# Kernel optimization log

Hardware: AMD Instinct MI355X
Metric: run time of the kernel (lower is better)

## Reference

```python
import jax, jax.numpy as jnp
import numpy as np

V, H, B, T_ENC, S, T_DEC, G = 18000, 400, 16, 256, 30, 8, 3


def setup_inputs() -> dict:
    key = jax.random.key(0)
    ks = jax.random.split(key, 16)
    def n(k, shape, s=0.1):
        return jax.random.normal(k, shape, jnp.float32) * s
    return {
        'story': jax.random.randint(ks[0], (B, T_ENC), 0, V, dtype=jnp.int32),
        'target_batches': jax.random.randint(ks[1], (B, S, T_DEC), 0, V, dtype=jnp.int32),
        'emb': n(ks[2], (V, H)),
        'enc_Wih_f': n(ks[3], (3 * H, H)), 'enc_Whh_f': n(ks[4], (3 * H, H)),
        'enc_bih_f': jnp.zeros((3 * H,), jnp.float32), 'enc_bhh_f': jnp.zeros((3 * H,), jnp.float32),
        'enc_Wih_b': n(ks[5], (3 * H, H)), 'enc_Whh_b': n(ks[6], (3 * H, H)),
        'enc_bih_b': jnp.zeros((3 * H,), jnp.float32), 'enc_bhh_b': jnp.zeros((3 * H,), jnp.float32),
        'dec_Wih': n(ks[7], (3 * H, H)), 'dec_Whh': n(ks[8], (3 * H, H)),
        'dec_bih': jnp.zeros((3 * H,), jnp.float32), 'dec_bhh': jnp.zeros((3 * H,), jnp.float32),
        'W_ratio': n(ks[9], (1, 3 * H)), 'b_ratio': jnp.zeros((1,), jnp.float32),
        'W_gate': n(ks[10], (G, H)), 'b_gate': jnp.zeros((G,), jnp.float32),
        'slot_emb': n(ks[11], (S, H)),
    }


def _gru_step(h, x, Wih, Whh, bih, bhh):
    # PyTorch GRU gate order: r, z, n
    gi = x @ Wih.T + bih
    gh = h @ Whh.T + bhh
    ir, iz, ig = jnp.split(gi, 3, axis=-1)
    hr, hz, hg = jnp.split(gh, 3, axis=-1)
    r = jax.nn.sigmoid(ir + hr)
    z = jax.nn.sigmoid(iz + hz)
    g = jnp.tanh(ig + r * hg)
    return (1.0 - z) * g + z * h


def _run_gru(xs, h0, Wih, Whh, bih, bhh):
    def step(h, x):
        h2 = _gru_step(h, x, Wih, Whh, bih, bhh)
        return h2, h2
    hT, out = jax.lax.scan(step, h0, xs)
    return out, hT


def reference(story, target_batches, emb,
              enc_Wih_f, enc_Whh_f, enc_bih_f, enc_bhh_f,
              enc_Wih_b, enc_Whh_b, enc_bih_b, enc_bhh_b,
              dec_Wih, dec_Whh, dec_bih, dec_bhh,
              W_ratio, b_ratio, W_gate, b_gate, slot_emb):
    # ---- EncoderRNN (bidirectional 1-layer GRU; dropout=0 / eval mode) ----
    x = emb[story.T]                       # (T_enc, B, H)
    h0 = jnp.zeros((B, H), x.dtype)
    out_f, h_f = _run_gru(x, h0, enc_Wih_f, enc_Whh_f, enc_bih_f, enc_bhh_f)
    out_b_rev, h_b = _run_gru(x[::-1], h0, enc_Wih_b, enc_Whh_b, enc_bih_b, enc_bhh_b)
    out_b = out_b_rev[::-1]
    enc_out = jnp.transpose(out_f + out_b, (1, 0, 2))   # (B, T_enc, H) = fwd+bwd halves summed
    enc_hidden = h_f + h_b                               # (B, H)     = hidden[0] + hidden[1]

    # ---- Generator decode loop ----
    SB = S * B
    dec_in0 = jnp.broadcast_to(slot_emb[:, None, :], (S, B, H)).reshape(SB, H)
    h = jnp.tile(enc_hidden, (S, 1))                     # (SB, H)
    enc_tiled = jnp.tile(enc_out, (S, 1, 1))             # (SB, T_enc, H)
    story_tiled = jnp.tile(story, (S, 1))                # (SB, T_enc)
    rows = jnp.arange(SB)[:, None]
    # teacher-forcing tokens per step, slot-major flatten to (T_dec, SB)
    tf_tokens = jnp.transpose(target_batches, (2, 1, 0)).reshape(T_DEC, SB)

    def step(carry, tok):
        h, dec_in = carry
        h2 = _gru_step(h, dec_in, dec_Wih, dec_Whh, dec_bih, dec_bhh)  # dec_state == new hidden
        scores = jnp.einsum('nd,ntd->nt', h2, enc_tiled)               # attend (all lens == T_enc)
        prob = jax.nn.softmax(scores, axis=1)
        context = jnp.einsum('nt,ntd->nd', prob, enc_tiled)
        gate = context @ W_gate.T + b_gate                              # (SB, G)
        p_vocab = jax.nn.softmax(h2 @ emb.T, axis=1)                    # (SB, V)
        p_gen = jnp.concatenate([h2, context, dec_in], axis=-1)         # (SB, 3H)
        sw = jax.nn.sigmoid(p_gen @ W_ratio.T + b_ratio)                # (SB, 1)
        ptr = jnp.zeros((SB, V), prob.dtype).at[rows, story_tiled].add(prob)  # scatter_add copy dist
        final = (1.0 - sw) * ptr + sw * p_vocab
        dec_in_next = emb[tok]                                          # teacher forcing
        return (h2, dec_in_next), (final, gate)

    _, (finals, gates) = jax.lax.scan(step, (h, dec_in0), tf_tokens)
    all_pointer_outputs = finals.reshape(T_DEC, S, B, V).transpose(1, 2, 0, 3)  # (S, B, T_dec, V)
    all_gate_outputs = gates[0].reshape(S, B, G)                                 # gate from step 0
    return all_pointer_outputs, all_gate_outputs
```

## Files before the change

kernel.cpp:

```cpp
#include <hip/hip_runtime.h>
#include <cstdint>
#include <cstddef>

#define VV 18000
#define HH 400
#define H3 1200
#define H3P 1280
#define KP 416
#define BB 16
#define TE 256
#define SS 30
#define TDN 8
#define GGN 3
#define SBN 480
#define NROW_ENC 4096
#define VP 18048
#define MP_DEC 512

#define EBLK 25

typedef __bf16 bf16;
typedef __attribute__((ext_vector_type(8))) __bf16 bf16x8;
typedef __attribute__((ext_vector_type(4))) float f32x4;
typedef __attribute__((ext_vector_type(4))) unsigned int u32x4;

static __device__ __forceinline__ float sigf(float x) {
    return 1.0f / (1.0f + __expf(-x));
}

__global__ __launch_bounds__(256) void gemm_bt(const bf16* __restrict__ A,
                                               const bf16* __restrict__ B,
                                               float* __restrict__ C,
                                               int M, int N, int K) {
    __shared__ __align__(16) bf16 sA[128 * 32];
    __shared__ __align__(16) bf16 sB[128 * 32];
    const int tid = threadIdx.x;
    const int lane = tid & 63;
    const int wave = tid >> 6;
    const int wm = wave >> 1, wn = wave & 1;
    const int m0 = blockIdx.x * 128, n0 = blockIdx.y * 128;
    f32x4 acc[4][4] = {};
    const int c0 = tid, c1 = tid + 256;
    const int r0 = c0 >> 2, q0 = (c0 & 3) * 8;
    const int r1 = c1 >> 2, q1 = (c1 & 3) * 8;
    const int ar = lane & 15, ak = (lane >> 4) * 8;
    const int nk = K >> 5;
    for (int kt = 0; kt < nk; ++kt) {
        const int kb = kt * 32;
        uint4 a0 = *(const uint4*)(A + (size_t)(m0 + r0) * K + kb + q0);
        uint4 a1 = *(const uint4*)(A + (size_t)(m0 + r1) * K + kb + q1);
        uint4 b0 = *(const uint4*)(B + (size_t)(n0 + r0) * K + kb + q0);
        uint4 b1 = *(const uint4*)(B + (size_t)(n0 + r1) * K + kb + q1);
        __syncthreads();
        *(uint4*)(sA + r0 * 32 + q0) = a0;
        *(uint4*)(sA + r1 * 32 + q1) = a1;
        *(uint4*)(sB + r0 * 32 + q0) = b0;
        *(uint4*)(sB + r1 * 32 + q1) = b1;
        __syncthreads();
        bf16x8 af[4], bg[4];
#pragma unroll
        for (int i = 0; i < 4; ++i)
            af[i] = *(const bf16x8*)(sA + (wm * 64 + i * 16 + ar) * 32 + ak);
#pragma unroll
        for (int j = 0; j < 4; ++j)
            bg[j] = *(const bf16x8*)(sB + (wn * 64 + j * 16 + ar) * 32 + ak);
#pragma unroll
        for (int i = 0; i < 4; ++i)
#pragma unroll
            for (int j = 0; j < 4; ++j)
                acc[i][j] = __builtin_amdgcn_mfma_f32_16x16x32_bf16(af[i], bg[j], acc[i][j], 0, 0, 0);
    }
    const int cr = (lane >> 4) * 4, cc = lane & 15;
#pragma unroll
    for (int i = 0; i < 4; ++i)
#pragma unroll
        for (int j = 0; j < 4; ++j)
#pragma unroll
            for (int q = 0; q < 4; ++q) {
                int row = m0 + wm * 64 + i * 16 + cr + q;
                int col = n0 + wn * 64 + j * 16 + cc;
                C[(size_t)row * N + col] = acc[i][j][q];
            }
}

__global__ void prep_pad_bf16(const float* __restrict__ src, bf16* __restrict__ dst,
                              int rows_real, int cols_real, int rows_pad, int cols_pad) {
    int idx = blockIdx.x * blockDim.x + threadIdx.x;
    int total = rows_pad * cols_pad;
    if (idx >= total) return;
    int r = idx / cols_pad, c = idx % cols_pad;
    float v = (r < rows_real && c < cols_real) ? src[(size_t)r * cols_real + c] : 0.f;
    dst[idx] = (bf16)v;
}

__global__ void prep_aenc(const int* __restrict__ story, const float* __restrict__ emb,
                          bf16* __restrict__ dst) {
    int idx = blockIdx.x * blockDim.x + threadIdx.x;
    if (idx >= NROW_ENC * KP) return;
    int m = idx / KP, k = idx % KP;
    int t = m >> 4, b = m & 15;
    float v = 0.f;
    if (k < HH) {
        int tok = story[b * TE + t];
        v = emb[(size_t)tok * HH + k];
    }
    dst[idx] = (bf16)v;
}

__global__ void prep_decx(const int* __restrict__ target, const float* __restrict__ emb,
                          const float* __restrict__ slot, float* __restrict__ xf,
                          bf16* __restrict__ xb) {
    int idx = blockIdx.x * blockDim.x + threadIdx.x;
    if (idx >= TDN * SBN * KP) return;
    int k = idx % KP;
    int nn = idx / KP;
    int n = nn % SBN;
    int td = nn / SBN;
    int s = n >> 4, b = n & 15;
    float v = 0.f;
    if (k < HH) {
        if (td == 0) v = slot[s * HH + k];
        else {
            int tok = target[(b * SS + s) * TDN + (td - 1)];
            v = emb[(size_t)tok * HH + k];
        }
        xf[((size_t)td * SBN + n) * HH + k] = v;
    }
    xb[idx] = (bf16)v;
}

__global__ void zero_bf16k(bf16* dst, int total) {
    int idx = blockIdx.x * blockDim.x + threadIdx.x;
    if (idx < total) dst[idx] = (bf16)0.f;
}

__global__ __launch_bounds__(256) void enc_rnn5(
    const float* __restrict__ gi_f, const float* __restrict__ gi_b,
    const float* __restrict__ whh_f, const float* __restrict__ whh_b,
    const float* __restrict__ bih_f, const float* __restrict__ bhh_f,
    const float* __restrict__ bih_b, const float* __restrict__ bhh_b,
    float* __restrict__ hist_f, float* __restrict__ hist_b,
    unsigned int* __restrict__ hbuf_f, unsigned int* __restrict__ hbuf_b,
    int* __restrict__ cnt) {
    const int dir = blockIdx.x & 1;
    const int blk = blockIdx.x >> 1;
    const int j0 = blk * 16;
    const float* gi  = dir ? gi_b : gi_f;
    const float* whh = dir ? whh_b : whh_f;
    const float* bih = dir ? bih_b : bih_f;
    const float* bhh = dir ? bhh_b : bhh_f;
    float* hist = dir ? hist_b : hist_f;
    unsigned int* hbuf = dir ? hbuf_b : hbuf_f;
    int* mycnt = cnt + dir * TE;

    __shared__ float GHL[3 * 256];

    const int tid = threadIdx.x;
    const int wv = tid >> 6, lane = tid & 63;

    const int ub = tid >> 4, ucol = tid & 15;
    const int uj = j0 + ucol;
    const float bihr = bih[uj], bihz = bih[HH + uj], bihg = bih[2 * HH + uj];
    const float bhhr = bhh[uj], bhhz = bhh[HH + uj], bhhg = bhh[2 * HH + uj];

    const int kk0 = (lane >> 4) * 8;
    bf16x8 Bf[13];
    if (wv < 3) {
        const int brow = wv * HH + j0 + (lane & 15);
#pragma unroll
        for (int ks = 0; ks < 13; ++ks) {
            bf16x8 v;
#pragma unroll
            for (int e = 0; e < 8; ++e) {
                int k = kk0 + ks * 32 + e;
                v[e] = (k < HH) ? (bf16)whh[(size_t)brow * HH + k] : (bf16)0.f;
            }
            Bf[ks] = v;
        }
    }

    union UV { unsigned int d[4]; bf16x8 v; };

    float hp = 0.f;

    for (int s = 0; s < TE; ++s) {
        const int tt = dir ? (TE - 1 - s) : s;
        const float* gir = gi + ((size_t)tt * BB + ub) * H3P;
        float gi0 = gir[uj];
        float gi1 = gir[HH + uj];
        float gi2 = gir[2 * HH + uj];

        f32x4 acc0 = {}, acc1 = {};
        if (s > 0) {
            if (tid == 0) {
                while (__hip_atomic_load(&mycnt[s - 1], __ATOMIC_RELAXED,
                                         __HIP_MEMORY_SCOPE_AGENT) < EBLK)
                    __builtin_amdgcn_s_sleep(1);
            }
            __syncthreads();
            if (wv < 3) {
                const int ttp = dir ? (tt + 1) : (tt - 1);
                const unsigned int* hrow =
                    hbuf + ((size_t)ttp * BB + (lane & 15)) * KP + kk0;
                u32x4 u[13][2];
#pragma unroll
                for (int ks = 0; ks < 13; ++ks) {
                    asm volatile("global_load_dwordx4 %0, %1, off sc0 sc1"
                                 : "=v"(u[ks][0]) : "v"(hrow + ks * 32));
                    asm volatile("global_load_dwordx4 %0, %1, off sc0 sc1"
                                 : "=v"(u[ks][1]) : "v"(hrow + ks * 32 + 4));
                }
                asm volatile("s_waitcnt vmcnt(0)" ::: "memory");
                __builtin_amdgcn_sched_barrier(0);
#pragma unroll
                for (int ks = 0; ks < 13; ++ks) {
                    u32x4 a = u[ks][0], b = u[ks][1];
                    UV ah, al;
                    ah.d[0] = (a.x & 0xffffu) | (a.y << 16);
                    ah.d[1] = (a.z & 0xffffu) | (a.w << 16);
                    ah.d[2] = (b.x & 0xffffu) | (b.y << 16);
                    ah.d[3] = (b.z & 0xffffu) | (b.w << 16);
                    al.d[0] = (a.x >> 16) | (a.y & 0xffff0000u);
                    al.d[1] = (a.z >> 16) | (a.w & 0xffff0000u);
                    al.d[2] = (b.x >> 16) | (b.y & 0xffff0000u);
                    al.d[3] = (b.z >> 16) | (b.w & 0xffff0000u);
                    acc0 = __builtin_amdgcn_mfma_f32_16x16x32_bf16(ah.v, Bf[ks], acc0, 0, 0, 0);
                    acc1 = __builtin_amdgcn_mfma_f32_16x16x32_bf16(al.v, Bf[ks], acc1, 0, 0, 0);
                }
            }
        }
        if (wv < 3) {
            f32x4 at = acc0 + acc1;
            const int cb0 = wv * 256 + ((lane >> 4) * 4) * 16 + (lane & 15);
            GHL[cb0]      = at[0];
            GHL[cb0 + 16] = at[1];
            GHL[cb0 + 32] = at[2];
            GHL[cb0 + 48] = at[3];
        }
        __syncthreads();

        float ghr = GHL[tid];
        float ghz = GHL[256 + tid];
        float ghg = GHL[512 + tid];
        float r = sigf(gi0 + bihr + ghr + bhhr);
        float z = sigf(gi1 + bihz + ghz + bhhz);
        float g = tanhf(gi2 + bihg + r * (ghg + bhhg));
        float hn = (1.f - z) * g + z * hp;
        hp = hn;
        hist[((size_t)tt * BB + ub) * HH + uj] = hn;
        bf16 hi = (bf16)hn;
        bf16 lo = (bf16)(hn - (float)hi);
        unsigned int pk = (unsigned int)__builtin_bit_cast(unsigned short, hi)
                        | ((unsigned int)__builtin_bit_cast(unsigned short, lo) << 16);
        unsigned int* hw = hbuf + ((size_t)tt * BB + ub) * KP + uj;
        asm volatile("global_store_dword %0, %1, off sc0 sc1" :: "v"(hw), "v"(pk) : "memory");

        asm volatile("s_waitcnt vmcnt(0)" ::: "memory");
        __syncthreads();
        if (tid == 0)
            __hip_atomic_fetch_add(&mycnt[s], 1, __ATOMIC_RELAXED, __HIP_MEMORY_SCOPE_AGENT);
    }
}

__global__ void combine_enc(const float* __restrict__ hf, const float* __restrict__ hb,
                            float* __restrict__ enc_out) {
    int idx = blockIdx.x * blockDim.x + threadIdx.x;
    if (idx >= BB * TE * HH) return;
    int hcol = idx % HH;
    int t = (idx / HH) % TE;
    int b = idx / (HH * TE);
    size_t src = ((size_t)t * BB + b) * HH + hcol;
    enc_out[idx] = hf[src] + hb[src];
}

__global__ void init_hdec(const float* __restrict__ hf, const float* __restrict__ hb,
                          float* __restrict__ hdec) {
    int idx = blockIdx.x * blockDim.x + threadIdx.x;
    if (idx >= SBN * HH) return;
    int hcol = idx % HH;
    int n = idx / HH;
    int b = n & 15;
    hdec[idx] = hf[((size_t)(TE - 1) * BB + b) * HH + hcol] + hb[((size_t)b) * HH + hcol];
}

__global__ void conv_h(const float* __restrict__ h, bf16* __restrict__ hb) {
    int idx = blockIdx.x * blockDim.x + threadIdx.x;
    if (idx >= SBN * HH) return;
    int n = idx / HH, k = idx % HH;
    hb[(size_t)n * KP + k] = (bf16)h[idx];
}

__global__ void gru_dec(const float* __restrict__ gi, const float* __restrict__ gh,
                        const float* __restrict__ bih, const float* __restrict__ bhh,
                        const float* __restrict__ hprev, float* __restrict__ hnew) {
    int idx = blockIdx.x * blockDim.x + threadIdx.x;
    if (idx >= SBN * HH) return;
    int n = idx / HH, j = idx % HH;
    const float* gir = gi + (size_t)n * H3P;
    const float* ghr = gh + (size_t)n * H3P;
    float r = sigf(gir[j] + bih[j] + ghr[j] + bhh[j]);
    float z = sigf(gir[HH + j] + bih[HH + j] + ghr[HH + j] + bhh[HH + j]);
    float g = tanhf(gir[2 * HH + j] + bih[2 * HH + j] + r * (ghr[2 * HH + j] + bhh[2 * HH + j]));
    hnew[idx] = (1.f - z) * g + z * hprev[idx];
}

__global__ __launch_bounds__(256) void attn(const float* __restrict__ h2,
                                            const float* __restrict__ enc,
                                            float* __restrict__ prob,
                                            float* __restrict__ ctx) {
    int n = blockIdx.x, b = n & 15, tid = threadIdx.x;
    __shared__ __align__(16) float hq[HH];
    __shared__ float sc[TE];
    __shared__ float red[4];
    for (int k = tid; k < HH; k += 256) hq[k] = h2[(size_t)n * HH + k];
    __syncthreads();
    const float4* er = (const float4*)(enc + ((size_t)b * TE + tid) * HH);
    const float4* hq4 = (const float4*)hq;
    float acc = 0.f;
#pragma unroll 4
    for (int k = 0; k < HH / 4; ++k) {
        float4 e = er[k];
        float4 hv = hq4[k];
        acc += e.x * hv.x + e.y * hv.y + e.z * hv.z + e.w * hv.w;
    }
    float m = acc;
    for (int d = 32; d; d >>= 1) m = fmaxf(m, __shfl_xor(m, d));
    if ((tid & 63) == 0) red[tid >> 6] = m;
    __syncthreads();
    m = fmaxf(fmaxf(red[0], red[1]), fmaxf(red[2], red[3]));
    __syncthreads();
    float e = __expf(acc - m);
    float ssum = e;
    for (int d = 32; d; d >>= 1) ssum += __shfl_xor(ssum, d);
    if ((tid & 63) == 0) red[tid >> 6] = ssum;
    __syncthreads();
    ssum = red[0] + red[1] + red[2] + red[3];
    float p = e / ssum;
    sc[tid] = p;
    prob[(size_t)n * TE + tid] = p;
    __syncthreads();
    for (int hcol = tid; hcol < HH; hcol += 256) {
        float a = 0.f;
        for (int t = 0; t < TE; ++t) a += sc[t] * enc[((size_t)b * TE + t) * HH + hcol];
        ctx[(size_t)n * HH + hcol] = a;
    }
}

__global__ __launch_bounds__(64) void swgate(const float* __restrict__ h2,
                                             const float* __restrict__ ctx,
                                             const float* __restrict__ dx,
                                             const float* __restrict__ Wr, const float* __restrict__ br,
                                             const float* __restrict__ Wg, const float* __restrict__ bg,
                                             float* __restrict__ sw, float* __restrict__ outg,
                                             int isfirst) {
    int n = blockIdx.x, lane = threadIdx.x;
    float a = 0.f;
    for (int k = lane; k < H3; k += 64) {
        float v = (k < HH) ? h2[(size_t)n * HH + k]
                : (k < 2 * HH) ? ctx[(size_t)n * HH + (k - HH)]
                : dx[(size_t)n * HH + (k - 2 * HH)];
        a += v * Wr[k];
    }
    for (int d = 32; d; d >>= 1) a += __shfl_xor(a, d);
    if (lane == 0) sw[n] = sigf(a + br[0]);
    if (isfirst) {
        for (int g = 0; g < GGN; ++g) {
            float b2 = 0.f;
            for (int k = lane; k < HH; k += 64) b2 += ctx[(size_t)n * HH + k] * Wg[g * HH + k];
            for (int d = 32; d; d >>= 1) b2 += __shfl_xor(b2, d);
            if (lane == 0) outg[n * GGN + g] = b2 + bg[g];
        }
    }
}

__global__ __launch_bounds__(1024) void smax_final(const float* __restrict__ logits,
                                                   const float* __restrict__ sw,
                                                   float* __restrict__ out, int td) {
    int n = blockIdx.x, tid = threadIdx.x;
    __shared__ float red[16];
    __shared__ float bc[2];
    float v[18];
    float mx = -1e30f;
#pragma unroll
    for (int i = 0; i < 18; ++i) {
        int c = tid + (i << 10);
        v[i] = (c < VV) ? logits[(size_t)n * VP + c] : -1e30f;
        mx = fmaxf(mx, v[i]);
    }
    for (int d = 32; d; d >>= 1) mx = fmaxf(mx, __shfl_xor(mx, d));
    if ((tid & 63) == 0) red[tid >> 6] = mx;
    __syncthreads();
    if (tid == 0) {
        float m2 = red[0];
        for (int w = 1; w < 16; ++w) m2 = fmaxf(m2, red[w]);
        bc[0] = m2;
    }
    __syncthreads();
    mx = bc[0];
    float s = 0.f;
#pragma unroll
    for (int i = 0; i < 18; ++i) {
        int c = tid + (i << 10);
        if (c < VV) { v[i] = __expf(v[i] - mx); s += v[i]; }
    }
    for (int d = 32; d; d >>= 1) s += __shfl_xor(s, d);
    if ((tid & 63) == 0) red[tid >> 6] = s;
    __syncthreads();
    if (tid == 0) {
        float s2 = 0.f;
        for (int w = 0; w < 16; ++w) s2 += red[w];
        bc[1] = s2;
    }
    __syncthreads();
    float scale = sw[n] / bc[1];
    float* orow = out + ((size_t)n * TDN + td) * VV;
#pragma unroll
    for (int i = 0; i < 18; ++i) {
        int c = tid + (i << 10);
        if (c < VV) orow[c] = v[i] * scale;
    }
}

__global__ void scatter_ptr(const int* __restrict__ story, const float* __restrict__ prob,
                            const float* __restrict__ sw, float* __restrict__ out, int td) {
    int n = blockIdx.x, t = threadIdx.x, b = n & 15;
    int tok = story[b * TE + t];
    float val = (1.f - sw[n]) * prob[(size_t)n * TE + t];
    atomicAdd(out + ((size_t)n * TDN + td) * VV + tok, val);
}

static inline int cdiv(long long a, long long b) { return (int)((a + b - 1) / b); }

extern "C" void kernel_launch(void* const* d_in, const int* in_sizes, int n_in,
                              void* d_out, int out_size, void* d_ws, size_t ws_size,
                              hipStream_t stream) {
    const int*   story  = (const int*)d_in[0];
    const int*   target = (const int*)d_in[1];
    const float* emb    = (const float*)d_in[2];
    const float* wih_f  = (const float*)d_in[3];
    const float* whh_f  = (const float*)d_in[4];
    const float* bih_f  = (const float*)d_in[5];
    const float* bhh_f  = (const float*)d_in[6];
    const float* wih_b  = (const float*)d_in[7];
    const float* whh_b  = (const float*)d_in[8];
    const float* bih_b  = (const float*)d_in[9];
    const float* bhh_b  = (const float*)d_in[10];
    const float* dwih   = (const float*)d_in[11];
    const float* dwhh   = (const float*)d_in[12];
    const float* dbih   = (const float*)d_in[13];
    const float* dbhh   = (const float*)d_in[14];
    const float* wr     = (const float*)d_in[15];
    const float* brr    = (const float*)d_in[16];
    const float* wgg    = (const float*)d_in[17];
    const float* bgg    = (const float*)d_in[18];
    const float* slot   = (const float*)d_in[19];
    float* out = (float*)d_out;

    char* wsb = (char*)d_ws;
    size_t off = 0;
    auto alloc = [&](size_t bytes) -> char* {
        char* p = wsb + off;
        off = (off + bytes + 255) & ~(size_t)255;
        return p;
    };
    bf16*  embb  = (bf16*)alloc((size_t)VP * KP * 2);
    bf16*  aenc  = (bf16*)alloc((size_t)NROW_ENC * KP * 2);
    bf16*  wfb   = (bf16*)alloc((size_t)H3P * KP * 2);
    bf16*  wbb   = (bf16*)alloc((size_t)H3P * KP * 2);
    bf16*  dwihb = (bf16*)alloc((size_t)H3P * KP * 2);
    bf16*  dwhhb = (bf16*)alloc((size_t)H3P * KP * 2);
    bf16*  decxb = (bf16*)alloc((size_t)TDN * SBN * KP * 2);
    bf16*  h2b   = (bf16*)alloc((size_t)MP_DEC * KP * 2);
    unsigned int* hbuff = (unsigned int*)alloc((size_t)TE * BB * KP * 4);
    unsigned int* hbufb = (unsigned int*)alloc((size_t)TE * BB * KP * 4);
    float* gif   = (float*)alloc((size_t)NROW_ENC * H3P * 4);
    float* gib   = (float*)alloc((size_t)NROW_ENC * H3P * 4);
    float* gidec = (float*)alloc((size_t)TDN * SBN * H3P * 4);
    float* ghdec = (float*)alloc((size_t)MP_DEC * H3P * 4);
    float* histf = (float*)alloc((size_t)TE * BB * HH * 4);
    float* histb = (float*)alloc((size_t)TE * BB * HH * 4);
    float* encout= (float*)alloc((size_t)BB * TE * HH * 4);
    float* decxf = (float*)alloc((size_t)TDN * SBN * HH * 4);
    float* hA    = (float*)alloc((size_t)SBN * HH * 4);
    float* hB    = (float*)alloc((size_t)SBN * HH * 4);
    float* ctx   = (float*)alloc((size_t)SBN * HH * 4);
    float* probw = (float*)alloc((size_t)SBN * TE * 4);
    float* sww   = (float*)alloc((size_t)SBN * 4);
    float* logits= (float*)alloc((size_t)MP_DEC * VP * 4);
    int*   cnt   = (int*)alloc((size_t)2 * TE * 4);
    (void)ws_size; (void)in_sizes; (void)n_in; (void)out_size;

    (void)hipMemsetAsync(cnt, 0, (size_t)2 * TE * 4, stream);

    const int thr = 256;
    prep_pad_bf16<<<cdiv((long long)VP * KP, thr), thr, 0, stream>>>(emb, embb, VV, HH, VP, KP);
    prep_aenc<<<cdiv((long long)NROW_ENC * KP, thr), thr, 0, stream>>>(story, emb, aenc);
    prep_pad_bf16<<<cdiv((long long)H3P * KP, thr), thr, 0, stream>>>(wih_f, wfb, H3, HH, H3P, KP);
    prep_pad_bf16<<<cdiv((long long)H3P * KP, thr), thr, 0, stream>>>(wih_b, wbb, H3, HH, H3P, KP);
    prep_pad_bf16<<<cdiv((long long)H3P * KP, thr), thr, 0, stream>>>(dwih, dwihb, H3, HH, H3P, KP);
    prep_pad_bf16<<<cdiv((long long)H3P * KP, thr), thr, 0, stream>>>(dwhh, dwhhb, H3, HH, H3P, KP);
    prep_decx<<<cdiv((long long)TDN * SBN * KP, thr), thr, 0, stream>>>(target, emb, slot, decxf, decxb);
    zero_bf16k<<<cdiv((long long)MP_DEC * KP, thr), thr, 0, stream>>>(h2b, MP_DEC * KP);

    {
        dim3 g(NROW_ENC / 128, H3P / 128);
        gemm_bt<<<g, 256, 0, stream>>>(aenc, wfb, gif, NROW_ENC, H3P, KP);
        gemm_bt<<<g, 256, 0, stream>>>(aenc, wbb, gib, NROW_ENC, H3P, KP);
    }
    {
        dim3 g((TDN * SBN) / 128, H3P / 128);
        gemm_bt<<<g, 256, 0, stream>>>(decxb, dwihb, gidec, TDN * SBN, H3P, KP);
    }

    enc_rnn5<<<2 * EBLK, 256, 0, stream>>>(gif, gib, whh_f, whh_b,
                                           bih_f, bhh_f, bih_b, bhh_b,
                                           histf, histb, hbuff, hbufb, cnt);

    combine_enc<<<cdiv((long long)BB * TE * HH, thr), thr, 0, stream>>>(histf, histb, encout);
    init_hdec<<<cdiv((long long)SBN * HH, thr), thr, 0, stream>>>(histf, histb, hA);

    float* hc = hA;
    float* hn = hB;
    for (int td = 0; td < TDN; ++td) {
        conv_h<<<cdiv((long long)SBN * HH, thr), thr, 0, stream>>>(hc, h2b);
        {
            dim3 g(MP_DEC / 128, H3P / 128);
            gemm_bt<<<g, 256, 0, stream>>>(h2b, dwhhb, ghdec, MP_DEC, H3P, KP);
        }
        gru_dec<<<cdiv((long long)SBN * HH, thr), thr, 0, stream>>>(
            gidec + (size_t)td * SBN * H3P, ghdec, dbih, dbhh, hc, hn);
        conv_h<<<cdiv((long long)SBN * HH, thr), thr, 0, stream>>>(hn, h2b);
        attn<<<SBN, 256, 0, stream>>>(hn, encout, probw, ctx);
        swgate<<<SBN, 64, 0, stream>>>(hn, ctx, decxf + (size_t)td * SBN * HH,
                                       wr, brr, wgg, bgg, sww,
                                       out + (size_t)SBN * TDN * VV, td == 0 ? 1 : 0);
        {
            dim3 g(MP_DEC / 128, VP / 128);
            gemm_bt<<<g, 256, 0, stream>>>(h2b, embb, logits, MP_DEC, VP, KP);
        }
        smax_final<<<SBN, 1024, 0, stream>>>(logits, sww, out, td);
        scatter_ptr<<<SBN, TE, 0, stream>>>(story, probw, sww, out, td);
        float* tmp = hc; hc = hn; hn = tmp;
    }
}
```

Measured before the change: 2.025 ms.

## Replace counter-based cross-block sync with sentinel-polling on hidden-state buffer

The encoder recurrence kernel stops using a per-step atomic counter plus spin-wait to sync blocks. Instead the hidden-state exchange buffers are pre-filled with an all-ones sentinel, and each wave polls its own data loads until no sentinel remains. This removes the store-drain wait, the block barrier, the atomic increment and the separate flag poll from each of the 256 serial steps, folding sync into the data read. It relies on a packed hi/lo bf16 word never equalling 0xFFFFFFFF (a NaN pattern) and adds two large memsets of the buffers.

Measured after the change: 2.233 ms. 1.1x slower.

```diff
diff --git a/kernel.cpp b/kernel.cpp
--- a/kernel.cpp
+++ b/kernel.cpp
@@ -18,6 +18,7 @@
 #define MP_DEC 512
 
 #define EBLK 25
+#define SENT 0xFFFFFFFFu
 
 typedef __bf16 bf16;
 typedef __attribute__((ext_vector_type(8))) __bf16 bf16x8;
@@ -26,6 +27,14 @@
 
 static __device__ __forceinline__ float sigf(float x) {
     return 1.0f / (1.0f + __expf(-x));
+}
+
+static __device__ __forceinline__ unsigned umax4(unsigned m, u32x4 v) {
+    m = m > v.x ? m : v.x;
+    m = m > v.y ? m : v.y;
+    m = m > v.z ? m : v.z;
+    m = m > v.w ? m : v.w;
+    return m;
 }
 
 __global__ __launch_bounds__(256) void gemm_bt(const bf16* __restrict__ A,
@@ -134,14 +143,13 @@
     if (idx < total) dst[idx] = (bf16)0.f;
 }
 
-__global__ __launch_bounds__(256) void enc_rnn5(
+__global__ __launch_bounds__(256) void enc_rnn7(
     const float* __restrict__ gi_f, const float* __restrict__ gi_b,
     const float* __restrict__ whh_f, const float* __restrict__ whh_b,
     const float* __restrict__ bih_f, const float* __restrict__ bhh_f,
     const float* __restrict__ bih_b, const float* __restrict__ bhh_b,
     float* __restrict__ hist_f, float* __restrict__ hist_b,
-    unsigned int* __restrict__ hbuf_f, unsigned int* __restrict__ hbuf_b,
-    int* __restrict__ cnt) {
+    unsigned int* __restrict__ hbuf_f, unsigned int* __restrict__ hbuf_b) {
     const int dir = blockIdx.x & 1;
     const int blk = blockIdx.x >> 1;
     const int j0 = blk * 16;
@@ -151,7 +159,6 @@
     const float* bhh = dir ? bhh_b : bhh_f;
     float* hist = dir ? hist_b : hist_f;
     unsigned int* hbuf = dir ? hbuf_b : hbuf_f;
-    int* mycnt = cnt + dir * TE;
 
     __shared__ float GHL[3 * 256];
 
@@ -164,6 +171,7 @@
     const float bhhr = bhh[uj], bhhz = bhh[HH + uj], bhhg = bhh[2 * HH + uj];
 
     const int kk0 = (lane >> 4) * 8;
+    const bool padlane = (kk0 >= 16);
     bf16x8 Bf[13];
     if (wv < 3) {
         const int brow = wv * HH + j0 + (lane & 15);
@@ -180,6 +188,7 @@
     }
 
     union UV { unsigned int d[4]; bf16x8 v; };
+    const u32x4 zz = {0u, 0u, 0u, 0u};
 
     float hp = 0.f;
 
@@ -191,42 +200,49 @@
         float gi2 = gir[2 * HH + uj];
 
         f32x4 acc0 = {}, acc1 = {};
-        if (s > 0) {
-            if (tid == 0) {
-                while (__hip_atomic_load(&mycnt[s - 1], __ATOMIC_RELAXED,
-                                         __HIP_MEMORY_SCOPE_AGENT) < EBLK)
-                    __builtin_amdgcn_s_sleep(1);
-            }
-            __syncthreads();
-            if (wv < 3) {
-                const int ttp = dir ? (tt + 1) : (tt - 1);
-                const unsigned int* hrow =
-                    hbuf + ((size_t)ttp * BB + (lane & 15)) * KP + kk0;
-                u32x4 u[13][2];
+        if (s > 0 && wv < 3) {
+            const int ttp = dir ? (tt + 1) : (tt - 1);
+            const unsigned int* hrow =
+                hbuf + ((size_t)ttp * BB + (lane & 15)) * KP + kk0;
+            u32x4 ua[13], ubv[13];
+            while (true) {
 #pragma unroll
                 for (int ks = 0; ks < 13; ++ks) {
-                    asm volatile("global_load_dwordx4 %0, %1, off sc0 sc1"
-                                 : "=v"(u[ks][0]) : "v"(hrow + ks * 32));
-                    asm volatile("global_load_dwordx4 %0, %1, off sc0 sc1"
-                                 : "=v"(u[ks][1]) : "v"(hrow + ks * 32 + 4));
+                    asm volatile("global_load_dwordx4 %0, %1, off offset:%c2 sc0 sc1"
+                                 : "=v"(ua[ks]) : "v"(hrow), "n"(ks * 128));
+                    asm volatile("global_load_dwordx4 %0, %1, off offset:%c2 sc0 sc1"
+                                 : "=v"(ubv[ks]) : "v"(hrow), "n"(ks * 128 + 16));
                 }
                 asm volatile("s_waitcnt vmcnt(0)" ::: "memory");
                 __builtin_amdgcn_sched_barrier(0);
-#pragma unroll
-                for (int ks = 0; ks < 13; ++ks) {
-                    u32x4 a = u[ks][0], b = u[ks][1];
-                    UV ah, al;
-                    ah.d[0] = (a.x & 0xffffu) | (a.y << 16);
-                    ah.d[1] = (a.z & 0xffffu) | (a.w << 16);
-                    ah.d[2] = (b.x & 0xffffu) | (b.y << 16);
-                    ah.d[3] = (b.z & 0xffffu) | (b.w << 16);
-                    al.d[0] = (a.x >> 16) | (a.y & 0xffff0000u);
-                    al.d[1] = (a.z >> 16) | (a.w & 0xffff0000u);
-                    al.d[2] = (b.x >> 16) | (b.y & 0xffff0000u);
-                    al.d[3] = (b.z >> 16) | (b.w & 0xffff0000u);
-                    acc0 = __builtin_amdgcn_mfma_f32_16x16x32_bf16(ah.v, Bf[ks], acc0, 0, 0, 0);
-                    acc1 = __builtin_amdgcn_mfma_f32_16x16x32_bf16(al.v, Bf[ks], acc1, 0, 0, 0);
+                unsigned mx = 0u;
+#pragma unroll
+                for (int ks = 0; ks < 12; ++ks) {
+                    mx = umax4(mx, ua[ks]);
+                    mx = umax4(mx, ubv[ks]);
                 }
+                if (!padlane) {
+                    mx = umax4(mx, ua[12]);
+                    mx = umax4(mx, ubv[12]);
+                }
+                if (__all((int)(mx != SENT))) break;
+                __builtin_amdgcn_s_sleep(1);
+            }
+            if (padlane) { ua[12] = zz; ubv[12] = zz; }
+#pragma unroll
+            for (int ks = 0; ks < 13; ++ks) {
+                u32x4 a = ua[ks], b = ubv[ks];
+                UV ah, al;
+                ah.d[0] = (a.x & 0xffffu) | (a.y << 16);
+                ah.d[1] = (a.z & 0xffffu) | (a.w << 16);
+                ah.d[2] = (b.x & 0xffffu) | (b.y << 16);
+                ah.d[3] = (b.z & 0xffffu) | (b.w << 16);
+                al.d[0] = (a.x >> 16) | (a.y & 0xffff0000u);
+                al.d[1] = (a.z >> 16) | (a.w & 0xffff0000u);
+                al.d[2] = (b.x >> 16) | (b.y & 0xffff0000u);
+                al.d[3] = (b.z >> 16) | (b.w & 0xffff0000u);
+                acc0 = __builtin_amdgcn_mfma_f32_16x16x32_bf16(ah.v, Bf[ks], acc0, 0, 0, 0);
+                acc1 = __builtin_amdgcn_mfma_f32_16x16x32_bf16(al.v, Bf[ks], acc1, 0, 0, 0);
             }
         }
         if (wv < 3) {
@@ -255,10 +271,7 @@
         unsigned int* hw = hbuf + ((size_t)tt * BB + ub) * KP + uj;
         asm volatile("global_store_dword %0, %1, off sc0 sc1" :: "v"(hw), "v"(pk) : "memory");
 
-        asm volatile("s_waitcnt vmcnt(0)" ::: "memory");
-        __syncthreads();
-        if (tid == 0)
-            __hip_atomic_fetch_add(&mycnt[s], 1, __ATOMIC_RELAXED, __HIP_MEMORY_SCOPE_AGENT);
+        __builtin_amdgcn_s_barrier();
     }
 }
 
@@ -487,10 +500,10 @@
     float* probw = (float*)alloc((size_t)SBN * TE * 4);
     float* sww   = (float*)alloc((size_t)SBN * 4);
     float* logits= (float*)alloc((size_t)MP_DEC * VP * 4);
-    int*   cnt   = (int*)alloc((size_t)2 * TE * 4);
     (void)ws_size; (void)in_sizes; (void)n_in; (void)out_size;
 
-    (void)hipMemsetAsync(cnt, 0, (size_t)2 * TE * 4, stream);
+    (void)hipMemsetAsync(hbuff, 0xFF, (size_t)TE * BB * KP * 4, stream);
+    (void)hipMemsetAsync(hbufb, 0xFF, (size_t)TE * BB * KP * 4, stream);
 
     const int thr = 256;
     prep_pad_bf16<<<cdiv((long long)VP * KP, thr), thr, 0, stream>>>(emb, embb, VV, HH, VP, KP);
@@ -512,9 +525,9 @@
         gemm_bt<<<g, 256, 0, stream>>>(decxb, dwihb, gidec, TDN * SBN, H3P, KP);
     }
 
-    enc_rnn5<<<2 * EBLK, 256, 0, stream>>>(gif, gib, whh_f, whh_b,
+    enc_rnn7<<<2 * EBLK, 256, 0, stream>>>(gif, gib, whh_f, whh_b,
                                            bih_f, bhh_f, bih_b, bhh_b,
-                                           histf, histb, hbuff, hbufb, cnt);
+                                           histf, histb, hbuff, hbufb);
 
     combine_enc<<<cdiv((long long)BB * TE * HH, thr), thr, 0, stream>>>(histf, histb, encout);
     init_hdec<<<cdiv((long long)SBN * HH, thr), thr, 0, stream>>>(histf, histb, hA);
```

## Replace encoder atomic counter with per-block flags and fuse decoder small kernels

Applied to the files above, without the earlier changes.

The encoder recurrence barrier now has each block write its own flag per step, and one wavefront polls all 25 flags in parallel with a wave-wide vote. This replaces the atomic counter incremented by every block and polled by a single thread. The hidden-state loads use immediate offsets. In the decoder, the bf16 conversion of h is folded into init_hdec and gru_dec, and the sigmoid-ratio/gate computation is folded into the attention kernel, which removes three launches per decode step and the ctx round trip. The cost is a larger flag buffer to clear, and polling traffic that reads 25 flags per step instead of one counter.

Measured after the change: 1.957 ms. 3.3% less time.

```diff
diff --git a/kernel.cpp b/kernel.cpp
--- a/kernel.cpp
+++ b/kernel.cpp
@@ -134,14 +134,14 @@
     if (idx < total) dst[idx] = (bf16)0.f;
 }
 
-__global__ __launch_bounds__(256) void enc_rnn5(
+__global__ __launch_bounds__(256) void enc_rnn10(
     const float* __restrict__ gi_f, const float* __restrict__ gi_b,
     const float* __restrict__ whh_f, const float* __restrict__ whh_b,
     const float* __restrict__ bih_f, const float* __restrict__ bhh_f,
     const float* __restrict__ bih_b, const float* __restrict__ bhh_b,
     float* __restrict__ hist_f, float* __restrict__ hist_b,
     unsigned int* __restrict__ hbuf_f, unsigned int* __restrict__ hbuf_b,
-    int* __restrict__ cnt) {
+    unsigned int* __restrict__ flags) {
     const int dir = blockIdx.x & 1;
     const int blk = blockIdx.x >> 1;
     const int j0 = blk * 16;
@@ -151,7 +151,6 @@
     const float* bhh = dir ? bhh_b : bhh_f;
     float* hist = dir ? hist_b : hist_f;
     unsigned int* hbuf = dir ? hbuf_b : hbuf_f;
-    int* mycnt = cnt + dir * TE;
 
     __shared__ float GHL[3 * 256];
 
@@ -192,29 +191,35 @@
 
         f32x4 acc0 = {}, acc1 = {};
         if (s > 0) {
-            if (tid == 0) {
-                while (__hip_atomic_load(&mycnt[s - 1], __ATOMIC_RELAXED,
-                                         __HIP_MEMORY_SCOPE_AGENT) < EBLK)
-                    __builtin_amdgcn_s_sleep(1);
+            if (wv == 0) {
+                const unsigned int* fl = flags + ((size_t)dir * TE + (s - 1)) * 32;
+                while (true) {
+                    unsigned f = 1u;
+                    if (lane < EBLK)
+                        asm volatile("global_load_dword %0, %1, off sc0 sc1"
+                                     : "=v"(f) : "v"(fl + lane));
+                    asm volatile("s_waitcnt vmcnt(0)" ::: "memory");
+                    if (__all((int)(f != 0u))) break;
+                }
             }
             __syncthreads();
             if (wv < 3) {
                 const int ttp = dir ? (tt + 1) : (tt - 1);
                 const unsigned int* hrow =
                     hbuf + ((size_t)ttp * BB + (lane & 15)) * KP + kk0;
-                u32x4 u[13][2];
+                u32x4 ua[13], ubv[13];
 #pragma unroll
                 for (int ks = 0; ks < 13; ++ks) {
-                    asm volatile("global_load_dwordx4 %0, %1, off sc0 sc1"
-                                 : "=v"(u[ks][0]) : "v"(hrow + ks * 32));
-                    asm volatile("global_load_dwordx4 %0, %1, off sc0 sc1"
-                                 : "=v"(u[ks][1]) : "v"(hrow + ks * 32 + 4));
+                    asm volatile("global_load_dwordx4 %0, %1, off offset:%c2 sc0 sc1"
+                                 : "=v"(ua[ks]) : "v"(hrow), "n"(ks * 128));
+                    asm volatile("global_load_dwordx4 %0, %1, off offset:%c2 sc0 sc1"
+                                 : "=v"(ubv[ks]) : "v"(hrow), "n"(ks * 128 + 16));
                 }
                 asm volatile("s_waitcnt vmcnt(0)" ::: "memory");
                 __builtin_amdgcn_sched_barrier(0);
 #pragma unroll
                 for (int ks = 0; ks < 13; ++ks) {
-                    u32x4 a = u[ks][0], b = u[ks][1];
+                    u32x4 a = ua[ks], b = ubv[ks];
                     UV ah, al;
                     ah.d[0] = (a.x & 0xffffu) | (a.y << 16);
                     ah.d[1] = (a.z & 0xffffu) | (a.w << 16);
@@ -257,8 +262,11 @@
 
         asm volatile("s_waitcnt vmcnt(0)" ::: "memory");
         __syncthreads();
-        if (tid == 0)
-            __hip_atomic_fetch_add(&mycnt[s], 1, __ATOMIC_RELAXED, __HIP_MEMORY_SCOPE_AGENT);
+        if (tid == 0) {
+            unsigned int one = 1u;
+            unsigned int* fw = flags + ((size_t)dir * TE + s) * 32 + blk;
+            asm volatile("global_store_dword %0, %1, off sc0 sc1" :: "v"(fw), "v"(one) : "memory");
+        }
     }
 }
 
@@ -273,26 +281,22 @@
     enc_out[idx] = hf[src] + hb[src];
 }
 
-__global__ void init_hdec(const float* __restrict__ hf, const float* __restrict__ hb,
-                          float* __restrict__ hdec) {
+__global__ void init_hdec2(const float* __restrict__ hf, const float* __restrict__ hb,
+                           float* __restrict__ hdec, bf16* __restrict__ h2b) {
     int idx = blockIdx.x * blockDim.x + threadIdx.x;
     if (idx >= SBN * HH) return;
     int hcol = idx % HH;
     int n = idx / HH;
     int b = n & 15;
-    hdec[idx] = hf[((size_t)(TE - 1) * BB + b) * HH + hcol] + hb[((size_t)b) * HH + hcol];
-}
-
-__global__ void conv_h(const float* __restrict__ h, bf16* __restrict__ hb) {
-    int idx = blockIdx.x * blockDim.x + threadIdx.x;
-    if (idx >= SBN * HH) return;
-    int n = idx / HH, k = idx % HH;
-    hb[(size_t)n * KP + k] = (bf16)h[idx];
-}
-
-__global__ void gru_dec(const float* __restrict__ gi, const float* __restrict__ gh,
-                        const float* __restrict__ bih, const float* __restrict__ bhh,
-                        const float* __restrict__ hprev, float* __restrict__ hnew) {
+    float v = hf[((size_t)(TE - 1) * BB + b) * HH + hcol] + hb[((size_t)b) * HH + hcol];
+    hdec[idx] = v;
+    h2b[(size_t)n * KP + hcol] = (bf16)v;
+}
+
+__global__ void gru_dec2(const float* __restrict__ gi, const float* __restrict__ gh,
+                         const float* __restrict__ bih, const float* __restrict__ bhh,
+                         const float* __restrict__ hprev, float* __restrict__ hnew,
+                         bf16* __restrict__ h2b) {
     int idx = blockIdx.x * blockDim.x + threadIdx.x;
     if (idx >= SBN * HH) return;
     int n = idx / HH, j = idx % HH;
@@ -301,15 +305,22 @@
     float r = sigf(gir[j] + bih[j] + ghr[j] + bhh[j]);
     float z = sigf(gir[HH + j] + bih[HH + j] + ghr[HH + j] + bhh[HH + j]);
     float g = tanhf(gir[2 * HH + j] + bih[2 * HH + j] + r * (ghr[2 * HH + j] + bhh[2 * HH + j]));
-    hnew[idx] = (1.f - z) * g + z * hprev[idx];
-}
-
-__global__ __launch_bounds__(256) void attn(const float* __restrict__ h2,
-                                            const float* __restrict__ enc,
-                                            float* __restrict__ prob,
-                                            float* __restrict__ ctx) {
+    float hn = (1.f - z) * g + z * hprev[idx];
+    hnew[idx] = hn;
+    h2b[(size_t)n * KP + j] = (bf16)hn;
+}
+
+__global__ __launch_bounds__(256) void attn2(const float* __restrict__ h2,
+                                             const float* __restrict__ enc,
+                                             const float* __restrict__ dx,
+                                             const float* __restrict__ Wr, const float* __restrict__ br,
+                                             const float* __restrict__ Wg, const float* __restrict__ bg,
+                                             float* __restrict__ prob,
+                                             float* __restrict__ sw, float* __restrict__ outg,
+                                             int isfirst) {
     int n = blockIdx.x, b = n & 15, tid = threadIdx.x;
     __shared__ __align__(16) float hq[HH];
+    __shared__ __align__(16) float cx[HH];
     __shared__ float sc[TE];
     __shared__ float red[4];
     for (int k = tid; k < HH; k += 256) hq[k] = h2[(size_t)n * HH + k];
@@ -342,33 +353,30 @@
     for (int hcol = tid; hcol < HH; hcol += 256) {
         float a = 0.f;
         for (int t = 0; t < TE; ++t) a += sc[t] * enc[((size_t)b * TE + t) * HH + hcol];
-        ctx[(size_t)n * HH + hcol] = a;
-    }
-}
-
-__global__ __launch_bounds__(64) void swgate(const float* __restrict__ h2,
-                                             const float* __restrict__ ctx,
-                                             const float* __restrict__ dx,
-                                             const float* __restrict__ Wr, const float* __restrict__ br,
-                                             const float* __restrict__ Wg, const float* __restrict__ bg,
-                                             float* __restrict__ sw, float* __restrict__ outg,
-                                             int isfirst) {
-    int n = blockIdx.x, lane = threadIdx.x;
+        cx[hcol] = a;
+    }
+    __syncthreads();
     float a = 0.f;
-    for (int k = lane; k < H3; k += 64) {
-        float v = (k < HH) ? h2[(size_t)n * HH + k]
-                : (k < 2 * HH) ? ctx[(size_t)n * HH + (k - HH)]
+    for (int k = tid; k < H3; k += 256) {
+        float v = (k < HH) ? hq[k]
+                : (k < 2 * HH) ? cx[k - HH]
                 : dx[(size_t)n * HH + (k - 2 * HH)];
         a += v * Wr[k];
     }
     for (int d = 32; d; d >>= 1) a += __shfl_xor(a, d);
-    if (lane == 0) sw[n] = sigf(a + br[0]);
+    if ((tid & 63) == 0) red[tid >> 6] = a;
+    __syncthreads();
+    if (tid == 0) sw[n] = sigf(red[0] + red[1] + red[2] + red[3] + br[0]);
     if (isfirst) {
+#pragma unroll
         for (int g = 0; g < GGN; ++g) {
             float b2 = 0.f;
-            for (int k = lane; k < HH; k += 64) b2 += ctx[(size_t)n * HH + k] * Wg[g * HH + k];
+            for (int k = tid; k < HH; k += 256) b2 += cx[k] * Wg[g * HH + k];
             for (int d = 32; d; d >>= 1) b2 += __shfl_xor(b2, d);
-            if (lane == 0) outg[n * GGN + g] = b2 + bg[g];
+            __syncthreads();
+            if ((tid & 63) == 0) red[tid >> 6] = b2;
+            __syncthreads();
+            if (tid == 0) outg[n * GGN + g] = red[0] + red[1] + red[2] + red[3] + bg[g];
         }
     }
 }
@@ -473,6 +481,7 @@
     bf16*  h2b   = (bf16*)alloc((size_t)MP_DEC * KP * 2);
     unsigned int* hbuff = (unsigned int*)alloc((size_t)TE * BB * KP * 4);
     unsigned int* hbufb = (unsigned int*)alloc((size_t)TE * BB * KP * 4);
+    unsigned int* flags = (unsigned int*)alloc((size_t)2 * TE * 32 * 4);
     float* gif   = (float*)alloc((size_t)NROW_ENC * H3P * 4);
     float* gib   = (float*)alloc((size_t)NROW_ENC * H3P * 4);
     float* gidec = (float*)alloc((size_t)TDN * SBN * H3P * 4);
@@ -483,14 +492,12 @@
     float* decxf = (float*)alloc((size_t)TDN * SBN * HH * 4);
     float* hA    = (float*)alloc((size_t)SBN * HH * 4);
     float* hB    = (float*)alloc((size_t)SBN * HH * 4);
-    float* ctx   = (float*)alloc((size_t)SBN * HH * 4);
     float* probw = (float*)alloc((size_t)SBN * TE * 4);
     float* sww   = (float*)alloc((size_t)SBN * 4);
     float* logits= (float*)alloc((size_t)MP_DEC * VP * 4);
-    int*   cnt   = (int*)alloc((size_t)2 * TE * 4);
     (void)ws_size; (void)in_sizes; (void)n_in; (void)out_size;
 
-    (void)hipMemsetAsync(cnt, 0, (size_t)2 * TE * 4, stream);
+    (void)hipMemsetAsync(flags, 0, (size_t)2 * TE * 32 * 4, stream);
 
     const int thr = 256;
     prep_pad_bf16<<<cdiv((long long)VP * KP, thr), thr, 0, stream>>>(emb, embb, VV, HH, VP, KP);
@@ -512,27 +519,24 @@
         gemm_bt<<<g, 256, 0, stream>>>(decxb, dwihb, gidec, TDN * SBN, H3P, KP);
     }
 
-    enc_rnn5<<<2 * EBLK, 256, 0, stream>>>(gif, gib, whh_f, whh_b,
-                                           bih_f, bhh_f, bih_b, bhh_b,
-                                           histf, histb, hbuff, hbufb, cnt);
+    enc_rnn10<<<2 * EBLK, 256, 0, stream>>>(gif, gib, whh_f, whh_b,
+                                            bih_f, bhh_f, bih_b, bhh_b,
+                                            histf, histb, hbuff, hbufb, flags);
 
     combine_enc<<<cdiv((long long)BB * TE * HH, thr), thr, 0, stream>>>(histf, histb, encout);
-    init_hdec<<<cdiv((long long)SBN * HH, thr), thr, 0, stream>>>(histf, histb, hA);
+    init_hdec2<<<cdiv((long long)SBN * HH, thr), thr, 0, stream>>>(histf, histb, hA, h2b);
 
     float* hc = hA;
     float* hn = hB;
     for (int td = 0; td < TDN; ++td) {
-        conv_h<<<cdiv((long long)SBN * HH, thr), thr, 0, stream>>>(hc, h2b);
         {
             dim3 g(MP_DEC / 128, H3P / 128);
             gemm_bt<<<g, 256, 0, stream>>>(h2b, dwhhb, ghdec, MP_DEC, H3P, KP);
         }
-        gru_dec<<<cdiv((long long)SBN * HH, thr), thr, 0, stream>>>(
-            gidec + (size_t)td * SBN * H3P, ghdec, dbih, dbhh, hc, hn);
-        conv_h<<<cdiv((long long)SBN * HH, thr), thr, 0, stream>>>(hn, h2b);
-        attn<<<SBN, 256, 0, stream>>>(hn, encout, probw, ctx);
-        swgate<<<SBN, 64, 0, stream>>>(hn, ctx, decxf + (size_t)td * SBN * HH,
-                                       wr, brr, wgg, bgg, sww,
+        gru_dec2<<<cdiv((long long)SBN * HH, thr), thr, 0, stream>>>(
+            gidec + (size_t)td * SBN * H3P, ghdec, dbih, dbhh, hc, hn, h2b);
+        attn2<<<SBN, 256, 0, stream>>>(hn, encout, decxf + (size_t)td * SBN * HH,
+                                       wr, brr, wgg, bgg, probw, sww,
                                        out + (size_t)SBN * TDN * VV, td == 0 ? 1 : 0);
         {
             dim3 g(MP_DEC / 128, VP / 128);
```
